# Optimization experiments

Hardware: AMD Instinct MI355X
Metric: run time of the kernel (lower is better)

Reference implementation:

```python
import jax, jax.numpy as jnp
import numpy as np

B, P = 4, 65536
TD, HID, OUT = 32, 128, 4
RES = 256
NFREQ = 6
CD = 3 * 2 * NFREQ  # frequency encoding out dim


def setup_inputs() -> dict:
    key = jax.random.key(0)
    ks = jax.random.split(key, 12)

    def w(k, shape):
        fan_in = shape[-1]
        return jax.random.normal(k, shape, jnp.float32) / np.sqrt(fan_in)

    return {
        "triplane": jax.random.normal(ks[0], (3 * B, TD, RES, RES), jnp.float32),
        "coords": jax.random.uniform(ks[1], (B, P, 3), jnp.float32),  # inside aabb [-1,1]^3
        "w_in": w(ks[2], (HID, TD + CD)),
        "b_in": jnp.zeros((HID,), jnp.float32),
        "w_skip": w(ks[3], (HID, TD + CD)),
        "b_skip": jnp.zeros((HID,), jnp.float32),
        "w_before": w(ks[4], (2, HID, HID)),
        "b_before": jnp.zeros((2, HID), jnp.float32),
        "w_after": w(ks[5], (2, HID, HID)),
        "b_after": jnp.zeros((2, HID), jnp.float32),
        "w_out": w(ks[6], (OUT, HID)),
        "b_out": jnp.zeros((OUT,), jnp.float32),
    }


@jax.custom_vjp
def trunc_exp(x):
    return jnp.exp(x)


def _trunc_exp_fwd(x):
    return jnp.exp(x), x


def _trunc_exp_bwd(x, g):
    return (g * jnp.exp(jnp.clip(x, -15.0, 15.0)),)


trunc_exp.defvjp(_trunc_exp_fwd, _trunc_exp_bwd)


def grid_sample_bilinear(feat, gx, gy):
    # feat: [N, C, H, W]; gx, gy: [N, Q] in [-1, 1]; align_corners=True, zero padding.
    N, C, H, W = feat.shape
    ix = (gx + 1.0) * 0.5 * (W - 1)
    iy = (gy + 1.0) * 0.5 * (H - 1)
    x0 = jnp.floor(ix)
    y0 = jnp.floor(iy)
    wx1 = ix - x0
    wy1 = iy - y0
    feat_flat = feat.reshape(N, C, H * W)

    def gather(xf, yf):
        xi = xf.astype(jnp.int32)
        yi = yf.astype(jnp.int32)
        valid = ((xi >= 0) & (xi < W) & (yi >= 0) & (yi < H)).astype(feat.dtype)
        xi = jnp.clip(xi, 0, W - 1)
        yi = jnp.clip(yi, 0, H - 1)
        idx = yi * W + xi  # [N, Q]
        g = jnp.take_along_axis(feat_flat, idx[:, None, :], axis=2)  # [N, C, Q]
        return g * valid[:, None, :]

    out = (
        gather(x0, y0) * ((1 - wx1) * (1 - wy1))[:, None, :]
        + gather(x0 + 1, y0) * (wx1 * (1 - wy1))[:, None, :]
        + gather(x0, y0 + 1) * ((1 - wx1) * wy1)[:, None, :]
        + gather(x0 + 1, y0 + 1) * (wx1 * wy1)[:, None, :]
    )
    return out  # [N, C, Q]


def freq_encode(x):
    # x: [B, P, 3] in [0, 1]; NeRF-style frequency encoding (tcnn 'Frequency').
    freqs = (2.0 ** jnp.arange(NFREQ, dtype=x.dtype)) * jnp.pi  # [NFREQ]
    ang = x[..., :, None] * freqs  # [B, P, 3, NFREQ]
    enc = jnp.concatenate([jnp.sin(ang), jnp.cos(ang)], axis=-1)  # [B, P, 3, 2*NFREQ]
    return enc.reshape(x.shape[0], x.shape[1], CD)


def reference(triplane, coords, w_in, b_in, w_skip, b_skip, w_before, b_before,
              w_after, b_after, w_out, b_out):
    aabb_min = jnp.full((3,), -1.0, jnp.float32)
    aabb_max = jnp.full((3,), 1.0, jnp.float32)

    scaled = 2.0 * (coords - aabb_min) / (aabb_max - aabb_min) - 1.0  # [-1,1]
    norm = (coords - aabb_min) / (aabb_max - aabb_min)  # [0,1]
    selector = jnp.all((norm > 0.0) & (norm < 1.0), axis=-1)  # [B, P]

    # planes: xy=(x,y), xz=(x,z), zy=(y,z); stacked per batch -> [3B, P, 2]
    coords_xy = scaled[:, :, (0, 1)]
    coords_xz = scaled[:, :, (0, 2)]
    coords_zy = scaled[:, :, (1, 2)]
    grid = jnp.stack([coords_xy, coords_xz, coords_zy], axis=1).reshape(3 * B, P, 2)

    feats = grid_sample_bilinear(triplane, grid[..., 0], grid[..., 1])  # [3B, TD, P]
    feats = feats.transpose(0, 2, 1).reshape(B, 3, P, TD).sum(axis=1)  # [B, P, TD]

    h = jnp.concatenate([freq_encode(norm), feats], axis=-1)  # [B, P, CD+TD]

    lin = lambda x, w, b: jnp.einsum("bpf,hf->bph", x, w) + b
    x = jax.nn.relu(lin(h, w_in, b_in))
    for i in range(w_before.shape[0]):
        x = jax.nn.relu(lin(x, w_before[i], b_before[i]))
    x = x + jax.nn.relu(lin(h, w_skip, b_skip))
    for i in range(w_after.shape[0]):
        x = jax.nn.relu(lin(x, w_after[i], b_after[i]))
    x = lin(x, w_out, b_out)  # [B, P, 4]

    rgb = jax.nn.sigmoid(x[..., :3])
    density = trunc_exp(x[..., 3:4] - 1.0) * selector[..., None].astype(x.dtype)
    return rgb, density
```

## Files before the change

kernel.cpp:

```cpp
#include <hip/hip_runtime.h>
#include <stdint.h>

typedef short short8 __attribute__((ext_vector_type(8)));
typedef float floatx16 __attribute__((ext_vector_type(16)));
typedef unsigned int uint32;

#define NPTS (4 * 65536)
#define RGB_OFF (NPTS * 3)

__device__ __forceinline__ uint16_t bf_rne(float f) {
  uint32 u = __float_as_uint(f);
  u += 0x7FFFu + ((u >> 16) & 1u);
  return (uint16_t)(u >> 16);
}
__device__ __forceinline__ uint32 pack2(float a, float b) {
  return __builtin_amdgcn_perm(__float_as_uint(b) + 0x8000u,
                               __float_as_uint(a) + 0x8000u, 0x07060302u);
}
__device__ __forceinline__ float bf_lo(uint32 u) { return __uint_as_float(u << 16); }
__device__ __forceinline__ float bf_hi(uint32 u) { return __uint_as_float(u & 0xFFFF0000u); }
__device__ __forceinline__ void swap32(uint32& a, uint32& b) {
  asm("v_permlane32_swap_b32 %0, %1" : "+v"(a), "+v"(b));
}
__device__ __forceinline__ void gacc(const uint16_t* p, float w, float* acc) {
  uint4 q = *(const uint4*)p;
  acc[0] += w * bf_lo(q.x);
  acc[1] += w * bf_hi(q.x);
  acc[2] += w * bf_lo(q.y);
  acc[3] += w * bf_hi(q.y);
  acc[4] += w * bf_lo(q.z);
  acc[5] += w * bf_hi(q.z);
  acc[6] += w * bf_lo(q.w);
  acc[7] += w * bf_hi(q.w);
}

__global__ __launch_bounds__(256) void k_tr(const float* __restrict__ tri,
                                            uint16_t* __restrict__ out) {
  __shared__ uint16_t tile[32 * 258];
  const int blk = blockIdx.x;
  const int n = blk >> 8, y = blk & 255;
  const int t = threadIdx.x;
  for (int c = 0; c < 32; ++c) {
    float v = tri[((size_t)(n * 32 + c)) * 65536 + y * 256 + t];
    tile[c * 258 + t] = bf_rne(v);
  }
  __syncthreads();
  uint16_t* dst = out + ((size_t)(n * 256 + y)) * 256 * 32;
  const int c0 = (t & 7) * 4;
  for (int i = 0; i < 8; ++i) {
    int x = (t >> 3) + 32 * i;
    uint32 d0 = (uint32)tile[(c0 + 0) * 258 + x] | ((uint32)tile[(c0 + 1) * 258 + x] << 16);
    uint32 d1 = (uint32)tile[(c0 + 2) * 258 + x] | ((uint32)tile[(c0 + 3) * 258 + x] << 16);
    *(uint2*)(dst + x * 32 + c0) = make_uint2(d0, d1);
  }
}

__global__ __launch_bounds__(256) void k_pack(
    const float* __restrict__ w_in, const float* __restrict__ w_skip,
    const float* __restrict__ w_before, const float* __restrict__ w_after,
    const float* __restrict__ w_out, const float* __restrict__ b_in,
    const float* __restrict__ b_skip, const float* __restrict__ b_before,
    const float* __restrict__ b_after, const float* __restrict__ b_out,
    uint16_t* __restrict__ wpack, float* __restrict__ bpack) {
  const int blk = blockIdx.x;
  if (blk >= 44) {
    for (int t = threadIdx.x; t < 800; t += 256) {
      int l, idx;
      if (t < 768) { l = t >> 7; idx = t & 127; }
      else { l = 6; idx = t - 768; }
      int mt = idx >> 5, rem = idx & 31;
      int half = rem >> 4, r = rem & 15;
      int f = mt * 32 + (r & 3) + 8 * (r >> 2) + 4 * half;
      float v;
      switch (l) {
        case 0: v = b_in[f]; break;
        case 1: v = b_before[f]; break;
        case 2: v = b_before[128 + f]; break;
        case 3: v = b_skip[f]; break;
        case 4: v = b_after[f]; break;
        case 5: v = b_after[128 + f]; break;
        default: v = (f < 4) ? b_out[f] : 0.0f; break;
      }
      bpack[l * 128 + idx] = v;
    }
    return;
  }
  const int w = blk * 4 + (threadIdx.x >> 6);
  const int L = threadIdx.x & 63;
  int lay, mt, k;
  if (w < 20)      { lay = 0; mt = w / 5;        k = w - mt * 5; }
  else if (w < 52) { int u = w - 20;  lay = 1; mt = u >> 3; k = u & 7; }
  else if (w < 84) { int u = w - 52;  lay = 2; mt = u >> 3; k = u & 7; }
  else if (w < 104){ int u = w - 84;  lay = 3; mt = u / 5;  k = u - mt * 5; }
  else if (w < 136){ int u = w - 104; lay = 4; mt = u >> 3; k = u & 7; }
  else if (w < 168){ int u = w - 136; lay = 5; mt = u >> 3; k = u & 7; }
  else             { lay = 6; mt = 0; k = w - 168; }
  const float* W;
  int insk = 0;
  switch (lay) {
    case 0: W = w_in; insk = 1; break;
    case 1: W = w_before; break;
    case 2: W = w_before + 16384; break;
    case 3: W = w_skip; insk = 1; break;
    case 4: W = w_after; break;
    case 5: W = w_after + 16384; break;
    default: W = w_out; break;
  }
  const int frow = mt * 32 + (L & 31);
  const int kbase = k * 16 + (L >> 5) * 8;
  uint16_t h[8];
#pragma unroll
  for (int j = 0; j < 8; ++j) {
    int kl = kbase + j;
    float v;
    if (insk) {
      int col = (kl < 32) ? (36 + kl) : ((kl < 68) ? (kl - 32) : -1);
      v = (col < 0) ? 0.0f : W[frow * 68 + col];
    } else if (lay == 6) {
      v = (frow < 4) ? W[frow * 128 + kl] : 0.0f;
    } else {
      v = W[frow * 128 + kl];
    }
    h[j] = bf_rne(v);
  }
  uint4 q;
  q.x = (uint32)h[0] | ((uint32)h[1] << 16);
  q.y = (uint32)h[2] | ((uint32)h[3] << 16);
  q.z = (uint32)h[4] | ((uint32)h[5] << 16);
  q.w = (uint32)h[6] | ((uint32)h[7] << 16);
  *(uint4*)(wpack + (size_t)w * 512 + L * 8) = q;
}


template <int LAY, int Ks, int FOFF>
__device__ __forceinline__ void mfma_block(floatx16* a, const short8* bin,
                                           const uint16_t* __restrict__ wpack,
                                           const float* __restrict__ bpack, int L,
                                           int kh) {
#pragma unroll
  for (int mt = 0; mt < 4; ++mt) {
    const float4* bp = (const float4*)(bpack + LAY * 128 + mt * 32 + kh * 16);
#pragma unroll
    for (int g = 0; g < 4; ++g) {
      float4 v = bp[g];
      a[mt][4 * g + 0] = v.x; a[mt][4 * g + 1] = v.y;
      a[mt][4 * g + 2] = v.z; a[mt][4 * g + 3] = v.w;
    }
  }
  const uint16_t* wp = wpack + (size_t)FOFF * 512 + L * 8;
#pragma unroll
  for (int k = 0; k < Ks; ++k) {
    short8 w0 = *(const short8*)(wp + (size_t)(0 * Ks + k) * 512);
    short8 w1 = *(const short8*)(wp + (size_t)(1 * Ks + k) * 512);
    short8 w2 = *(const short8*)(wp + (size_t)(2 * Ks + k) * 512);
    short8 w3 = *(const short8*)(wp + (size_t)(3 * Ks + k) * 512);
    a[0] = __builtin_amdgcn_mfma_f32_32x32x16_bf16(w0, bin[k], a[0], 0, 0, 0);
    a[1] = __builtin_amdgcn_mfma_f32_32x32x16_bf16(w1, bin[k], a[1], 0, 0, 0);
    a[2] = __builtin_amdgcn_mfma_f32_32x32x16_bf16(w2, bin[k], a[2], 0, 0, 0);
    a[3] = __builtin_amdgcn_mfma_f32_32x32x16_bf16(w3, bin[k], a[3], 0, 0, 0);
  }
}

template <int LAY, int Ks, int FOFF>
__device__ __forceinline__ void layer_dense(const short8* bin, short8* bout,
                                            const uint16_t* __restrict__ wpack,
                                            const float* __restrict__ bpack, int L,
                                            int kh) {
  floatx16 a[4];
  mfma_block<LAY, Ks, FOFF>(a, bin, wpack, bpack, L, kh);
#pragma unroll
  for (int f = 0; f < 8; ++f) {
    const int mt = f >> 1, s = f & 1;
    uint32 q0a = pack2(fmaxf(a[mt][8 * s + 0], 0.f), fmaxf(a[mt][8 * s + 1], 0.f));
    uint32 q0b = pack2(fmaxf(a[mt][8 * s + 2], 0.f), fmaxf(a[mt][8 * s + 3], 0.f));
    uint32 q1a = pack2(fmaxf(a[mt][8 * s + 4], 0.f), fmaxf(a[mt][8 * s + 5], 0.f));
    uint32 q1b = pack2(fmaxf(a[mt][8 * s + 6], 0.f), fmaxf(a[mt][8 * s + 7], 0.f));
    swap32(q0a, q1a);
    swap32(q0b, q1b);
    bout[f] = __builtin_bit_cast(short8, make_uint4(q0a, q0b, q1a, q1b));
  }
}

template <int LAY, int Ks, int FOFF>
__device__ __forceinline__ void layer_skip(const short8* hin, short8* bio,
                                           const uint16_t* __restrict__ wpack,
                                           const float* __restrict__ bpack, int L,
                                           int kh) {
  floatx16 a[4];
  mfma_block<LAY, Ks, FOFF>(a, hin, wpack, bpack, L, kh);
#pragma unroll
  for (int f = 0; f < 8; ++f) {
    const int mt = f >> 1, s = f & 1;
    uint4 old = __builtin_bit_cast(uint4, bio[f]);
    uint32 uA = old.x, uB = old.y, uC = old.z, uD = old.w;
    swap32(uA, uC);
    swap32(uB, uD);
    float r0 = fmaxf(a[mt][8 * s + 0], 0.f) + bf_lo(uA);
    float r1 = fmaxf(a[mt][8 * s + 1], 0.f) + bf_hi(uA);
    float r2 = fmaxf(a[mt][8 * s + 2], 0.f) + bf_lo(uB);
    float r3 = fmaxf(a[mt][8 * s + 3], 0.f) + bf_hi(uB);
    float r4 = fmaxf(a[mt][8 * s + 4], 0.f) + bf_lo(uC);
    float r5 = fmaxf(a[mt][8 * s + 5], 0.f) + bf_hi(uC);
    float r6 = fmaxf(a[mt][8 * s + 6], 0.f) + bf_lo(uD);
    float r7 = fmaxf(a[mt][8 * s + 7], 0.f) + bf_hi(uD);
    uint32 q0a = pack2(r0, r1), q0b = pack2(r2, r3);
    uint32 q1a = pack2(r4, r5), q1b = pack2(r6, r7);
    swap32(q0a, q1a);
    swap32(q0b, q1b);
    bio[f] = __builtin_bit_cast(short8, make_uint4(q0a, q0b, q1a, q1b));
  }
}

__global__ __launch_bounds__(256, 3) void k_main(
    const uint16_t* __restrict__ trit, const float* __restrict__ trif,
    const float* __restrict__ coords, const uint16_t* __restrict__ wpack,
    const float* __restrict__ bpack, float* __restrict__ dout, int fast) {
  const int t = threadIdx.x;
  const int L = t & 63;
  const int kh = L >> 5;
  const int p = (t >> 6) * 32 + (L & 31);
  const int pg = blockIdx.x * 128 + p;

  float cx = coords[pg * 3 + 0], cy = coords[pg * 3 + 1], cz = coords[pg * 3 + 2];
  float f1x = cx + 1.0f, f1y = cy + 1.0f, f1z = cz + 1.0f;
  float nx = f1x * 0.5f, ny = f1y * 0.5f, nz = f1z * 0.5f;
  float sx = f1x - 1.0f, sy = f1y - 1.0f, sz = f1z - 1.0f;
  bool sel = (nx > 0.f) & (nx < 1.f) & (ny > 0.f) & (ny < 1.f) & (nz > 0.f) & (nz < 1.f);
  const int b = pg >> 16;
  float acc[16];
#pragma unroll
  for (int j = 0; j < 16; ++j) acc[j] = 0.f;
#pragma unroll
  for (int pl = 0; pl < 3; ++pl) {
    float gx = (pl == 2) ? sy : sx;
    float gy = (pl == 0) ? sy : sz;
    float ix = ((gx + 1.0f) * 0.5f) * 255.0f;
    float iy = ((gy + 1.0f) * 0.5f) * 255.0f;
    float x0f = floorf(ix), y0f = floorf(iy);
    float wx = ix - x0f, wy = iy - y0f;
    float vx0 = (x0f >= 0.0f && x0f < 256.0f) ? 1.f : 0.f;
    float vx1 = (x0f >= -1.0f && x0f < 255.0f) ? 1.f : 0.f;
    float vy0 = (y0f >= 0.0f && y0f < 256.0f) ? 1.f : 0.f;
    float vy1 = (y0f >= -1.0f && y0f < 255.0f) ? 1.f : 0.f;
    int x0 = min(max((int)x0f, 0), 255), x1 = min(max((int)x0f + 1, 0), 255);
    int y0 = min(max((int)y0f, 0), 255), y1 = min(max((int)y0f + 1, 0), 255);
    float w00 = (1.f - wx) * (1.f - wy) * vx0 * vy0;
    float w10 = wx * (1.f - wy) * vx1 * vy0;
    float w01 = (1.f - wx) * wy * vx0 * vy1;
    float w11 = wx * wy * vx1 * vy1;
    const int n = 3 * b + pl;
    if (fast) {
      const uint16_t* cb = trit + ((size_t)n << 21) + kh * 8;
      size_t o00 = (size_t)(y0 * 256 + x0) << 5, o10 = (size_t)(y0 * 256 + x1) << 5;
      size_t o01 = (size_t)(y1 * 256 + x0) << 5, o11 = (size_t)(y1 * 256 + x1) << 5;
      gacc(cb + o00, w00, acc); gacc(cb + 16 + o00, w00, acc + 8);
      gacc(cb + o10, w10, acc); gacc(cb + 16 + o10, w10, acc + 8);
      gacc(cb + o01, w01, acc); gacc(cb + 16 + o01, w01, acc + 8);
      gacc(cb + o11, w11, acc); gacc(cb + 16 + o11, w11, acc + 8);
    } else {
      const float* basef = trif + (((size_t)n * 32) << 16);
#pragma unroll
      for (int j = 0; j < 8; ++j) {
        const float* c0p = basef + (((size_t)(kh * 8 + j)) << 16);
        const float* c1p = basef + (((size_t)(16 + kh * 8 + j)) << 16);
        acc[j] += w00 * c0p[y0 * 256 + x0] + w10 * c0p[y0 * 256 + x1] +
                  w01 * c0p[y1 * 256 + x0] + w11 * c0p[y1 * 256 + x1];
        acc[8 + j] += w00 * c1p[y0 * 256 + x0] + w10 * c1p[y0 * 256 + x1] +
                      w01 * c1p[y1 * 256 + x0] + w11 * c1p[y1 * 256 + x1];
      }
    }
  }
  short8 hf[5];
  hf[0] = __builtin_bit_cast(
      short8, make_uint4(pack2(acc[0], acc[1]), pack2(acc[2], acc[3]),
                         pack2(acc[4], acc[5]), pack2(acc[6], acc[7])));
  hf[1] = __builtin_bit_cast(
      short8, make_uint4(pack2(acc[8], acc[9]), pack2(acc[10], acc[11]),
                         pack2(acc[12], acc[13]), pack2(acc[14], acc[15])));
  {
    float sv[3][6], cv[3][6];
#pragma unroll
    for (int d = 0; d < 3; ++d) {
      float nd = (d == 0) ? nx : (d == 1) ? ny : nz;
#pragma unroll
      for (int k = 0; k < 6; ++k) {
        float rev = nd * (0.5f * (float)(1 << k));
        float r = rev - rintf(rev);
        sv[d][k] = __builtin_amdgcn_sinf(r);
        cv[d][k] = __builtin_amdgcn_cosf(r);
      }
    }
    if (kh == 0) {
      hf[2] = __builtin_bit_cast(
          short8, make_uint4(pack2(sv[0][0], sv[0][1]), pack2(sv[0][2], sv[0][3]),
                             pack2(sv[0][4], sv[0][5]), pack2(cv[0][0], cv[0][1])));
      hf[3] = __builtin_bit_cast(
          short8, make_uint4(pack2(sv[1][4], sv[1][5]), pack2(cv[1][0], cv[1][1]),
                             pack2(cv[1][2], cv[1][3]), pack2(cv[1][4], cv[1][5])));
      hf[4] = __builtin_bit_cast(
          short8, make_uint4(pack2(cv[2][2], cv[2][3]), pack2(cv[2][4], cv[2][5]), 0u, 0u));
    } else {
      hf[2] = __builtin_bit_cast(
          short8, make_uint4(pack2(cv[0][2], cv[0][3]), pack2(cv[0][4], cv[0][5]),
                             pack2(sv[1][0], sv[1][1]), pack2(sv[1][2], sv[1][3])));
      hf[3] = __builtin_bit_cast(
          short8, make_uint4(pack2(sv[2][0], sv[2][1]), pack2(sv[2][2], sv[2][3]),
                             pack2(sv[2][4], sv[2][5]), pack2(cv[2][0], cv[2][1])));
      hf[4] = __builtin_bit_cast(short8, make_uint4(0u, 0u, 0u, 0u));
    }
  }

  short8 bf[8];
  layer_dense<0, 5, 0>(hf, bf, wpack, bpack, L, kh);
  layer_dense<1, 8, 20>(bf, bf, wpack, bpack, L, kh);
  layer_dense<2, 8, 52>(bf, bf, wpack, bpack, L, kh);
  layer_skip<3, 5, 84>(hf, bf, wpack, bpack, L, kh);
  layer_dense<4, 8, 104>(bf, bf, wpack, bpack, L, kh);
  layer_dense<5, 8, 136>(bf, bf, wpack, bpack, L, kh);

  {
    floatx16 a;
    const float4* bp = (const float4*)(bpack + 768 + kh * 16);
#pragma unroll
    for (int g = 0; g < 4; ++g) {
      float4 v = bp[g];
      a[4 * g + 0] = v.x; a[4 * g + 1] = v.y; a[4 * g + 2] = v.z; a[4 * g + 3] = v.w;
    }
    const uint16_t* wp = wpack + (size_t)168 * 512 + L * 8;
#pragma unroll
    for (int k = 0; k < 8; ++k) {
      short8 af = *(const short8*)(wp + (size_t)k * 512);
      a = __builtin_amdgcn_mfma_f32_32x32x16_bf16(af, bf[k], a, 0, 0, 0);
    }
    if (kh == 0) {
      const float l2e = 1.44269504f;
      float r0 = 1.0f / (1.0f + exp2f(-l2e * a[0]));
      float r1 = 1.0f / (1.0f + exp2f(-l2e * a[1]));
      float r2 = 1.0f / (1.0f + exp2f(-l2e * a[2]));
      float dens = exp2f((a[3] - 1.0f) * l2e) * (sel ? 1.0f : 0.0f);
      dout[pg * 3 + 0] = r0;
      dout[pg * 3 + 1] = r1;
      dout[pg * 3 + 2] = r2;
      dout[RGB_OFF + pg] = dens;
    }
  }
}

extern "C" void kernel_launch(void* const* d_in, const int* in_sizes, int n_in,
                              void* d_out, int out_size, void* d_ws, size_t ws_size,
                              hipStream_t stream) {
  const float* tri = (const float*)d_in[0];
  const float* coords = (const float*)d_in[1];
  const float* w_in = (const float*)d_in[2];
  const float* b_in = (const float*)d_in[3];
  const float* w_skip = (const float*)d_in[4];
  const float* b_skip = (const float*)d_in[5];
  const float* w_bef = (const float*)d_in[6];
  const float* b_bef = (const float*)d_in[7];
  const float* w_aft = (const float*)d_in[8];
  const float* b_aft = (const float*)d_in[9];
  const float* w_out = (const float*)d_in[10];
  const float* b_out = (const float*)d_in[11];
  const size_t TRI_B = (size_t)12 * 256 * 256 * 32 * 2;
  const size_t WP_B = (size_t)176 * 1024;
  const size_t BP_B = 3200;
  char* ws = (char*)d_ws;
  const int fast = (ws_size >= TRI_B + WP_B + BP_B) ? 1 : 0;
  uint16_t* trit;
  uint16_t* wpk;
  float* bpk;
  if (fast) {
    trit = (uint16_t*)ws;
    wpk = (uint16_t*)(ws + TRI_B);
    bpk = (float*)(ws + TRI_B + WP_B);
  } else {
    trit = (uint16_t*)ws;
    wpk = (uint16_t*)ws;
    bpk = (float*)(ws + WP_B);
  }
  if (fast) k_tr<<<dim3(3072), dim3(256), 0, stream>>>(tri, trit);
  k_pack<<<dim3(45), dim3(256), 0, stream>>>(w_in, w_skip, w_bef, w_aft, w_out,
                                             b_in, b_skip, b_bef, b_aft, b_out,
                                             wpk, bpk);
  k_main<<<dim3(2048), dim3(256), 0, stream>>>(trit, tri, coords, wpk, bpk,
                                               (float*)d_out, fast);
}
```

Baseline: 272.2 us.

## Stage MLP weights through shared memory per layer and simplify triplane transpose

The main kernel now copies each layer's packed bf16 weights from global memory into a 32 KB shared buffer, with barriers between layers, and the MFMA loops read weight fragments from LDS instead of global or cache. The triplane transpose kernel drops its shared-memory tile: each thread gathers 32 channels with strided loads and writes 64 contiguous bytes. The goal is to cut repeated global or L2 weight traffic across waves and simplify the conversion. In exchange, the main kernel gains 12 block-wide barriers and 32 KB of LDS, which may limit occupancy and serialise the layers.

```diff
diff --git a/kernel.cpp b/kernel.cpp
--- a/kernel.cpp
+++ b/kernel.cpp
@@ -36,23 +36,22 @@
 
 __global__ __launch_bounds__(256) void k_tr(const float* __restrict__ tri,
                                             uint16_t* __restrict__ out) {
-  __shared__ uint16_t tile[32 * 258];
-  const int blk = blockIdx.x;
-  const int n = blk >> 8, y = blk & 255;
-  const int t = threadIdx.x;
-  for (int c = 0; c < 32; ++c) {
-    float v = tri[((size_t)(n * 32 + c)) * 65536 + y * 256 + t];
-    tile[c * 258 + t] = bf_rne(v);
-  }
-  __syncthreads();
-  uint16_t* dst = out + ((size_t)(n * 256 + y)) * 256 * 32;
-  const int c0 = (t & 7) * 4;
-  for (int i = 0; i < 8; ++i) {
-    int x = (t >> 3) + 32 * i;
-    uint32 d0 = (uint32)tile[(c0 + 0) * 258 + x] | ((uint32)tile[(c0 + 1) * 258 + x] << 16);
-    uint32 d1 = (uint32)tile[(c0 + 2) * 258 + x] | ((uint32)tile[(c0 + 3) * 258 + x] << 16);
-    *(uint2*)(dst + x * 32 + c0) = make_uint2(d0, d1);
-  }
+  const size_t P = (size_t)blockIdx.x * 256 + threadIdx.x;
+  const int n = (int)(P >> 16);
+  const int rem = (int)(P & 65535);
+  const float* src = tri + ((size_t)n << 21) + rem;
+  uint32 q[16];
+#pragma unroll
+  for (int c = 0; c < 16; ++c) {
+    float a = src[(size_t)(2 * c) << 16];
+    float b = src[(size_t)(2 * c + 1) << 16];
+    q[c] = pack2(a, b);
+  }
+  uint4* dst = (uint4*)(out + P * 32);
+  dst[0] = make_uint4(q[0], q[1], q[2], q[3]);
+  dst[1] = make_uint4(q[4], q[5], q[6], q[7]);
+  dst[2] = make_uint4(q[8], q[9], q[10], q[11]);
+  dst[3] = make_uint4(q[12], q[13], q[14], q[15]);
 }
 
 __global__ __launch_bounds__(256) void k_pack(
@@ -131,10 +130,20 @@
   *(uint4*)(wpack + (size_t)w * 512 + L * 8) = q;
 }
 
-
-template <int LAY, int Ks, int FOFF>
+template <int NFRAG>
+__device__ __forceinline__ void stage(const uint16_t* __restrict__ wp_base,
+                                      uint16_t* __restrict__ wbuf, int t) {
+#pragma unroll
+  for (int i = 0; i < NFRAG * 64 / 256; ++i) {
+    const int g = t + i * 256;
+    uint4 v = *(const uint4*)(wp_base + g * 8);
+    *(uint4*)(wbuf + g * 8) = v;
+  }
+}
+
+template <int LAY, int Ks>
 __device__ __forceinline__ void mfma_block(floatx16* a, const short8* bin,
-                                           const uint16_t* __restrict__ wpack,
+                                           const uint16_t* __restrict__ wbuf,
                                            const float* __restrict__ bpack, int L,
                                            int kh) {
 #pragma unroll
@@ -147,7 +156,7 @@
       a[mt][4 * g + 2] = v.z; a[mt][4 * g + 3] = v.w;
     }
   }
-  const uint16_t* wp = wpack + (size_t)FOFF * 512 + L * 8;
+  const uint16_t* wp = wbuf + L * 8;
 #pragma unroll
   for (int k = 0; k < Ks; ++k) {
     short8 w0 = *(const short8*)(wp + (size_t)(0 * Ks + k) * 512);
@@ -161,13 +170,13 @@
   }
 }
 
-template <int LAY, int Ks, int FOFF>
+template <int LAY, int Ks>
 __device__ __forceinline__ void layer_dense(const short8* bin, short8* bout,
-                                            const uint16_t* __restrict__ wpack,
+                                            const uint16_t* __restrict__ wbuf,
                                             const float* __restrict__ bpack, int L,
                                             int kh) {
   floatx16 a[4];
-  mfma_block<LAY, Ks, FOFF>(a, bin, wpack, bpack, L, kh);
+  mfma_block<LAY, Ks>(a, bin, wbuf, bpack, L, kh);
 #pragma unroll
   for (int f = 0; f < 8; ++f) {
     const int mt = f >> 1, s = f & 1;
@@ -181,13 +190,13 @@
   }
 }
 
-template <int LAY, int Ks, int FOFF>
+template <int LAY, int Ks>
 __device__ __forceinline__ void layer_skip(const short8* hin, short8* bio,
-                                           const uint16_t* __restrict__ wpack,
+                                           const uint16_t* __restrict__ wbuf,
                                            const float* __restrict__ bpack, int L,
                                            int kh) {
   floatx16 a[4];
-  mfma_block<LAY, Ks, FOFF>(a, hin, wpack, bpack, L, kh);
+  mfma_block<LAY, Ks>(a, hin, wbuf, bpack, L, kh);
 #pragma unroll
   for (int f = 0; f < 8; ++f) {
     const int mt = f >> 1, s = f & 1;
@@ -215,11 +224,14 @@
     const uint16_t* __restrict__ trit, const float* __restrict__ trif,
     const float* __restrict__ coords, const uint16_t* __restrict__ wpack,
     const float* __restrict__ bpack, float* __restrict__ dout, int fast) {
+  __shared__ __align__(16) uint16_t wbuf[16384];
   const int t = threadIdx.x;
   const int L = t & 63;
   const int kh = L >> 5;
   const int p = (t >> 6) * 32 + (L & 31);
   const int pg = blockIdx.x * 128 + p;
+
+  stage<20>(wpack, wbuf, t);
 
   float cx = coords[pg * 3 + 0], cy = coords[pg * 3 + 1], cz = coords[pg * 3 + 2];
   float f1x = cx + 1.0f, f1y = cy + 1.0f, f1z = cz + 1.0f;
@@ -311,12 +323,19 @@
   }
 
   short8 bf[8];
-  layer_dense<0, 5, 0>(hf, bf, wpack, bpack, L, kh);
-  layer_dense<1, 8, 20>(bf, bf, wpack, bpack, L, kh);
-  layer_dense<2, 8, 52>(bf, bf, wpack, bpack, L, kh);
-  layer_skip<3, 5, 84>(hf, bf, wpack, bpack, L, kh);
-  layer_dense<4, 8, 104>(bf, bf, wpack, bpack, L, kh);
-  layer_dense<5, 8, 136>(bf, bf, wpack, bpack, L, kh);
+  __syncthreads();
+  layer_dense<0, 5>(hf, bf, wbuf, bpack, L, kh);
+  __syncthreads(); stage<32>(wpack + (size_t)20 * 512, wbuf, t); __syncthreads();
+  layer_dense<1, 8>(bf, bf, wbuf, bpack, L, kh);
+  __syncthreads(); stage<32>(wpack + (size_t)52 * 512, wbuf, t); __syncthreads();
+  layer_dense<2, 8>(bf, bf, wbuf, bpack, L, kh);
+  __syncthreads(); stage<20>(wpack + (size_t)84 * 512, wbuf, t); __syncthreads();
+  layer_skip<3, 5>(hf, bf, wbuf, bpack, L, kh);
+  __syncthreads(); stage<32>(wpack + (size_t)104 * 512, wbuf, t); __syncthreads();
+  layer_dense<4, 8>(bf, bf, wbuf, bpack, L, kh);
+  __syncthreads(); stage<32>(wpack + (size_t)136 * 512, wbuf, t); __syncthreads();
+  layer_dense<5, 8>(bf, bf, wbuf, bpack, L, kh);
+  __syncthreads(); stage<8>(wpack + (size_t)168 * 512, wbuf, t); __syncthreads();
 
   {
     floatx16 a;
@@ -326,7 +345,7 @@
       float4 v = bp[g];
       a[4 * g + 0] = v.x; a[4 * g + 1] = v.y; a[4 * g + 2] = v.z; a[4 * g + 3] = v.w;
     }
-    const uint16_t* wp = wpack + (size_t)168 * 512 + L * 8;
+    const uint16_t* wp = wbuf + L * 8;
 #pragma unroll
     for (int k = 0; k < 8; ++k) {
       short8 af = *(const short8*)(wp + (size_t)k * 512);
```

Result: no change. 267.4 us (-1.8%).

## Spill input features to LDS, raise occupancy, and rewrite triplane transpose without shared tile

Applied to the files above, without the earlier changes.

The main kernel now stores the 40-wide input feature fragments in shared memory instead of holding them in registers across the MLP, which frees VGPRs so launch bounds can go from 3 to 4 blocks per CU. The fast/slow path flag becomes a template parameter so the unused branch is compiled out. The triplane transpose kernel is rewritten to have each thread read float4s from 32 channels and write contiguous 64-byte channel vectors directly, removing the LDS tile and barrier. The cost is extra LDS reads in the two layers that consume the input features, and higher register pressure in the transpose kernel.

```diff
diff --git a/kernel.cpp b/kernel.cpp
--- a/kernel.cpp
+++ b/kernel.cpp
@@ -36,23 +36,27 @@
 
 __global__ __launch_bounds__(256) void k_tr(const float* __restrict__ tri,
                                             uint16_t* __restrict__ out) {
-  __shared__ uint16_t tile[32 * 258];
-  const int blk = blockIdx.x;
-  const int n = blk >> 8, y = blk & 255;
-  const int t = threadIdx.x;
-  for (int c = 0; c < 32; ++c) {
-    float v = tri[((size_t)(n * 32 + c)) * 65536 + y * 256 + t];
-    tile[c * 258 + t] = bf_rne(v);
-  }
-  __syncthreads();
-  uint16_t* dst = out + ((size_t)(n * 256 + y)) * 256 * 32;
-  const int c0 = (t & 7) * 4;
-  for (int i = 0; i < 8; ++i) {
-    int x = (t >> 3) + 32 * i;
-    uint32 d0 = (uint32)tile[(c0 + 0) * 258 + x] | ((uint32)tile[(c0 + 1) * 258 + x] << 16);
-    uint32 d1 = (uint32)tile[(c0 + 2) * 258 + x] | ((uint32)tile[(c0 + 3) * 258 + x] << 16);
-    *(uint2*)(dst + x * 32 + c0) = make_uint2(d0, d1);
-  }
+  const size_t pix = ((size_t)blockIdx.x * 256 + threadIdx.x) * 4;
+  const int n = (int)(pix >> 16);
+  const int rem = (int)(pix & 65535);
+  const float* src = tri + ((size_t)n << 21) + rem;
+  uint32 q[4][16];
+#pragma unroll
+  for (int c = 0; c < 16; ++c) {
+    float4 a = *(const float4*)(src + ((size_t)(2 * c) << 16));
+    float4 b = *(const float4*)(src + ((size_t)(2 * c + 1) << 16));
+    q[0][c] = pack2(a.x, b.x);
+    q[1][c] = pack2(a.y, b.y);
+    q[2][c] = pack2(a.z, b.z);
+    q[3][c] = pack2(a.w, b.w);
+  }
+  uint4* dst = (uint4*)(out + pix * 32);
+#pragma unroll
+  for (int j = 0; j < 4; ++j)
+#pragma unroll
+    for (int g = 0; g < 4; ++g)
+      dst[j * 4 + g] =
+          make_uint4(q[j][4 * g], q[j][4 * g + 1], q[j][4 * g + 2], q[j][4 * g + 3]);
 }
 
 __global__ __launch_bounds__(256) void k_pack(
@@ -132,11 +136,8 @@
 }
 
 
-template <int LAY, int Ks, int FOFF>
-__device__ __forceinline__ void mfma_block(floatx16* a, const short8* bin,
-                                           const uint16_t* __restrict__ wpack,
-                                           const float* __restrict__ bpack, int L,
-                                           int kh) {
+__device__ __forceinline__ void bias_init(floatx16* a, const float* __restrict__ bpack,
+                                          int LAY, int kh) {
 #pragma unroll
   for (int mt = 0; mt < 4; ++mt) {
     const float4* bp = (const float4*)(bpack + LAY * 128 + mt * 32 + kh * 16);
@@ -147,27 +148,9 @@
       a[mt][4 * g + 2] = v.z; a[mt][4 * g + 3] = v.w;
     }
   }
-  const uint16_t* wp = wpack + (size_t)FOFF * 512 + L * 8;
-#pragma unroll
-  for (int k = 0; k < Ks; ++k) {
-    short8 w0 = *(const short8*)(wp + (size_t)(0 * Ks + k) * 512);
-    short8 w1 = *(const short8*)(wp + (size_t)(1 * Ks + k) * 512);
-    short8 w2 = *(const short8*)(wp + (size_t)(2 * Ks + k) * 512);
-    short8 w3 = *(const short8*)(wp + (size_t)(3 * Ks + k) * 512);
-    a[0] = __builtin_amdgcn_mfma_f32_32x32x16_bf16(w0, bin[k], a[0], 0, 0, 0);
-    a[1] = __builtin_amdgcn_mfma_f32_32x32x16_bf16(w1, bin[k], a[1], 0, 0, 0);
-    a[2] = __builtin_amdgcn_mfma_f32_32x32x16_bf16(w2, bin[k], a[2], 0, 0, 0);
-    a[3] = __builtin_amdgcn_mfma_f32_32x32x16_bf16(w3, bin[k], a[3], 0, 0, 0);
-  }
-}
-
-template <int LAY, int Ks, int FOFF>
-__device__ __forceinline__ void layer_dense(const short8* bin, short8* bout,
-                                            const uint16_t* __restrict__ wpack,
-                                            const float* __restrict__ bpack, int L,
-                                            int kh) {
-  floatx16 a[4];
-  mfma_block<LAY, Ks, FOFF>(a, bin, wpack, bpack, L, kh);
+}
+
+__device__ __forceinline__ void epi_dense(floatx16* a, short8* bout) {
 #pragma unroll
   for (int f = 0; f < 8; ++f) {
     const int mt = f >> 1, s = f & 1;
@@ -181,13 +164,7 @@
   }
 }
 
-template <int LAY, int Ks, int FOFF>
-__device__ __forceinline__ void layer_skip(const short8* hin, short8* bio,
-                                           const uint16_t* __restrict__ wpack,
-                                           const float* __restrict__ bpack, int L,
-                                           int kh) {
-  floatx16 a[4];
-  mfma_block<LAY, Ks, FOFF>(a, hin, wpack, bpack, L, kh);
+__device__ __forceinline__ void epi_skip(floatx16* a, short8* bio) {
 #pragma unroll
   for (int f = 0; f < 8; ++f) {
     const int mt = f >> 1, s = f & 1;
@@ -211,15 +188,64 @@
   }
 }
 
-__global__ __launch_bounds__(256, 3) void k_main(
+template <int LAY, int Ks, int FOFF>
+__device__ __forceinline__ void layer_dense(const short8* bin, short8* bout,
+                                            const uint16_t* __restrict__ wpack,
+                                            const float* __restrict__ bpack, int L,
+                                            int kh) {
+  floatx16 a[4];
+  bias_init(a, bpack, LAY, kh);
+  const uint16_t* wp = wpack + (size_t)FOFF * 512 + L * 8;
+#pragma unroll
+  for (int k = 0; k < Ks; ++k) {
+    short8 w0 = *(const short8*)(wp + (size_t)(0 * Ks + k) * 512);
+    short8 w1 = *(const short8*)(wp + (size_t)(1 * Ks + k) * 512);
+    short8 w2 = *(const short8*)(wp + (size_t)(2 * Ks + k) * 512);
+    short8 w3 = *(const short8*)(wp + (size_t)(3 * Ks + k) * 512);
+    a[0] = __builtin_amdgcn_mfma_f32_32x32x16_bf16(w0, bin[k], a[0], 0, 0, 0);
+    a[1] = __builtin_amdgcn_mfma_f32_32x32x16_bf16(w1, bin[k], a[1], 0, 0, 0);
+    a[2] = __builtin_amdgcn_mfma_f32_32x32x16_bf16(w2, bin[k], a[2], 0, 0, 0);
+    a[3] = __builtin_amdgcn_mfma_f32_32x32x16_bf16(w3, bin[k], a[3], 0, 0, 0);
+  }
+  epi_dense(a, bout);
+}
+
+template <int LAY, int Ks, int FOFF, bool SKIP>
+__device__ __forceinline__ void layer_h(const uint16_t* __restrict__ hl, short8* bio,
+                                        const uint16_t* __restrict__ wpack,
+                                        const float* __restrict__ bpack, int L,
+                                        int kh) {
+  floatx16 a[4];
+  bias_init(a, bpack, LAY, kh);
+  const uint16_t* wp = wpack + (size_t)FOFF * 512 + L * 8;
+#pragma unroll
+  for (int k = 0; k < Ks; ++k) {
+    short8 bk = *(const short8*)(hl + (size_t)k * 512);
+    short8 w0 = *(const short8*)(wp + (size_t)(0 * Ks + k) * 512);
+    short8 w1 = *(const short8*)(wp + (size_t)(1 * Ks + k) * 512);
+    short8 w2 = *(const short8*)(wp + (size_t)(2 * Ks + k) * 512);
+    short8 w3 = *(const short8*)(wp + (size_t)(3 * Ks + k) * 512);
+    a[0] = __builtin_amdgcn_mfma_f32_32x32x16_bf16(w0, bk, a[0], 0, 0, 0);
+    a[1] = __builtin_amdgcn_mfma_f32_32x32x16_bf16(w1, bk, a[1], 0, 0, 0);
+    a[2] = __builtin_amdgcn_mfma_f32_32x32x16_bf16(w2, bk, a[2], 0, 0, 0);
+    a[3] = __builtin_amdgcn_mfma_f32_32x32x16_bf16(w3, bk, a[3], 0, 0, 0);
+  }
+  if (SKIP) epi_skip(a, bio);
+  else epi_dense(a, bio);
+}
+
+template <int FAST>
+__global__ __launch_bounds__(256, 4) void k_main(
     const uint16_t* __restrict__ trit, const float* __restrict__ trif,
     const float* __restrict__ coords, const uint16_t* __restrict__ wpack,
-    const float* __restrict__ bpack, float* __restrict__ dout, int fast) {
+    const float* __restrict__ bpack, float* __restrict__ dout) {
+  __shared__ __align__(16) uint16_t hlds[4 * 5 * 64 * 8];
   const int t = threadIdx.x;
   const int L = t & 63;
   const int kh = L >> 5;
   const int p = (t >> 6) * 32 + (L & 31);
   const int pg = blockIdx.x * 128 + p;
+  uint16_t* hl = hlds + ((size_t)((t >> 6) * 5) * 64 + L) * 8;
 
   float cx = coords[pg * 3 + 0], cy = coords[pg * 3 + 1], cz = coords[pg * 3 + 2];
   float f1x = cx + 1.0f, f1y = cy + 1.0f, f1z = cz + 1.0f;
@@ -249,7 +275,7 @@
     float w01 = (1.f - wx) * wy * vx0 * vy1;
     float w11 = wx * wy * vx1 * vy1;
     const int n = 3 * b + pl;
-    if (fast) {
+    if (FAST) {
       const uint16_t* cb = trit + ((size_t)n << 21) + kh * 8;
       size_t o00 = (size_t)(y0 * 256 + x0) << 5, o10 = (size_t)(y0 * 256 + x1) << 5;
       size_t o01 = (size_t)(y1 * 256 + x0) << 5, o11 = (size_t)(y1 * 256 + x1) << 5;
@@ -270,13 +296,11 @@
       }
     }
   }
-  short8 hf[5];
-  hf[0] = __builtin_bit_cast(
-      short8, make_uint4(pack2(acc[0], acc[1]), pack2(acc[2], acc[3]),
-                         pack2(acc[4], acc[5]), pack2(acc[6], acc[7])));
-  hf[1] = __builtin_bit_cast(
-      short8, make_uint4(pack2(acc[8], acc[9]), pack2(acc[10], acc[11]),
-                         pack2(acc[12], acc[13]), pack2(acc[14], acc[15])));
+  *(uint4*)(hl + 0 * 512) = make_uint4(pack2(acc[0], acc[1]), pack2(acc[2], acc[3]),
+                                       pack2(acc[4], acc[5]), pack2(acc[6], acc[7]));
+  *(uint4*)(hl + 1 * 512) =
+      make_uint4(pack2(acc[8], acc[9]), pack2(acc[10], acc[11]),
+                 pack2(acc[12], acc[13]), pack2(acc[14], acc[15]));
   {
     float sv[3][6], cv[3][6];
 #pragma unroll
@@ -291,30 +315,30 @@
       }
     }
     if (kh == 0) {
-      hf[2] = __builtin_bit_cast(
-          short8, make_uint4(pack2(sv[0][0], sv[0][1]), pack2(sv[0][2], sv[0][3]),
-                             pack2(sv[0][4], sv[0][5]), pack2(cv[0][0], cv[0][1])));
-      hf[3] = __builtin_bit_cast(
-          short8, make_uint4(pack2(sv[1][4], sv[1][5]), pack2(cv[1][0], cv[1][1]),
-                             pack2(cv[1][2], cv[1][3]), pack2(cv[1][4], cv[1][5])));
-      hf[4] = __builtin_bit_cast(
-          short8, make_uint4(pack2(cv[2][2], cv[2][3]), pack2(cv[2][4], cv[2][5]), 0u, 0u));
+      *(uint4*)(hl + 2 * 512) =
+          make_uint4(pack2(sv[0][0], sv[0][1]), pack2(sv[0][2], sv[0][3]),
+                     pack2(sv[0][4], sv[0][5]), pack2(cv[0][0], cv[0][1]));
+      *(uint4*)(hl + 3 * 512) =
+          make_uint4(pack2(sv[1][4], sv[1][5]), pack2(cv[1][0], cv[1][1]),
+                     pack2(cv[1][2], cv[1][3]), pack2(cv[1][4], cv[1][5]));
+      *(uint4*)(hl + 4 * 512) =
+          make_uint4(pack2(cv[2][2], cv[2][3]), pack2(cv[2][4], cv[2][5]), 0u, 0u);
     } else {
-      hf[2] = __builtin_bit_cast(
-          short8, make_uint4(pack2(cv[0][2], cv[0][3]), pack2(cv[0][4], cv[0][5]),
-                             pack2(sv[1][0], sv[1][1]), pack2(sv[1][2], sv[1][3])));
-      hf[3] = __builtin_bit_cast(
-          short8, make_uint4(pack2(sv[2][0], sv[2][1]), pack2(sv[2][2], sv[2][3]),
-                             pack2(sv[2][4], sv[2][5]), pack2(cv[2][0], cv[2][1])));
-      hf[4] = __builtin_bit_cast(short8, make_uint4(0u, 0u, 0u, 0u));
+      *(uint4*)(hl + 2 * 512) =
+          make_uint4(pack2(cv[0][2], cv[0][3]), pack2(cv[0][4], cv[0][5]),
+                     pack2(sv[1][0], sv[1][1]), pack2(sv[1][2], sv[1][3]));
+      *(uint4*)(hl + 3 * 512) =
+          make_uint4(pack2(sv[2][0], sv[2][1]), pack2(sv[2][2], sv[2][3]),
+                     pack2(sv[2][4], sv[2][5]), pack2(cv[2][0], cv[2][1]));
+      *(uint4*)(hl + 4 * 512) = make_uint4(0u, 0u, 0u, 0u);
     }
   }
 
   short8 bf[8];
-  layer_dense<0, 5, 0>(hf, bf, wpack, bpack, L, kh);
+  layer_h<0, 5, 0, false>(hl, bf, wpack, bpack, L, kh);
   layer_dense<1, 8, 20>(bf, bf, wpack, bpack, L, kh);
   layer_dense<2, 8, 52>(bf, bf, wpack, bpack, L, kh);
-  layer_skip<3, 5, 84>(hf, bf, wpack, bpack, L, kh);
+  layer_h<3, 5, 84, true>(hl, bf, wpack, bpack, L, kh);
   layer_dense<4, 8, 104>(bf, bf, wpack, bpack, L, kh);
   layer_dense<5, 8, 136>(bf, bf, wpack, bpack, L, kh);
 
@@ -378,10 +402,14 @@
     wpk = (uint16_t*)ws;
     bpk = (float*)(ws + WP_B);
   }
-  if (fast) k_tr<<<dim3(3072), dim3(256), 0, stream>>>(tri, trit);
+  if (fast) k_tr<<<dim3(768), dim3(256), 0, stream>>>(tri, trit);
   k_pack<<<dim3(45), dim3(256), 0, stream>>>(w_in, w_skip, w_bef, w_aft, w_out,
                                              b_in, b_skip, b_bef, b_aft, b_out,
                                              wpk, bpk);
-  k_main<<<dim3(2048), dim3(256), 0, stream>>>(trit, tri, coords, wpk, bpk,
-                                               (float*)d_out, fast);
-}
+  if (fast)
+    k_main<1><<<dim3(2048), dim3(256), 0, stream>>>(trit, tri, coords, wpk, bpk,
+                                                    (float*)d_out);
+  else
+    k_main<0><<<dim3(2048), dim3(256), 0, stream>>>(trit, tri, coords, wpk, bpk,
+                                                    (float*)d_out);
+}
```

Measured after the change: 323.5 us. +18.8%, slower.
